# Kernel optimization log

Measured on AMD Instinct MI355X. Metric: run time of the kernel, lower is better.

## Reference

```python
import jax, jax.numpy as jnp
import numpy as np

SIGMA = 1.0
N_DOCS = 10_000_000
N_SAMPLED = 8192  # n = ceil(sqrt(random_pairs)), random_pairs = 67108864


def setup_inputs() -> dict:
    key = jax.random.key(0)
    k1, k2, k3 = jax.random.split(key, 3)
    scores = jax.random.normal(k1, (N_DOCS, 1), dtype=jnp.float32)
    target = jax.random.randint(k2, (N_DOCS,), 0, 5, dtype=jnp.int32)
    random_docs = jax.random.randint(k3, (N_SAMPLED,), 0, N_DOCS, dtype=jnp.int32)
    return {"scores": scores, "target": target, "random_docs": random_docs}


def reference(scores, target, random_docs):
    # Gather sampled docs' targets and scores.
    t = target[random_docs].astype(jnp.float32)   # [n]
    s = scores[random_docs, 0]                    # [n]
    # S_ij = sign(target_i - target_j)  (the if/elif/else ladder in the source)
    S = jnp.sign(t[:, None] - t[None, :])         # [n, n]
    # Source bug preserved: z_j = s_i.detach(), so calc_p(z_i, z_j) = sigmoid(0) = 0.5 exactly.
    # lambda_ij = sigma * (0.5 * (1 - S) - 0.5). (i == j pairs contribute 0 since S = 0.)
    lam = SIGMA * (0.5 * (1.0 - S) - 0.5)         # [n, n]
    row = jnp.sum(lam, axis=1)                    # sum_j lambda_ij for each sampled i
    # Source bug preserved: lambda_i is never reset across the outer loop -> cumulative sum.
    cum = jnp.cumsum(row)                         # [n]
    # loss = sum_k cum_lambda[k] * s_{i_k}; lambdas are detached (constants w.r.t. grad).
    loss = jnp.sum(jax.lax.stop_gradient(cum) * s)
    return loss.reshape(1)
```

## Files before the change

### kernel.cpp

```cpp
#include <hip/hip_runtime.h>

#define NS   8192
#define NB   64
#define T1   128
#define RECW 16

__device__ __forceinline__ unsigned fnv11(const unsigned* w, unsigned seed) {
    unsigned h = seed;
    #pragma unroll
    for (int i = 0; i < 11; ++i) h = (h ^ w[i]) * 16777619u;
    return h;
}

__global__ __launch_bounds__(T1) void k_fused(
    const float* __restrict__ scores,
    const int*   __restrict__ target,
    const int*   __restrict__ docs,
    unsigned*    __restrict__ ws,
    float*       __restrict__ out)
{
    const int tid  = threadIdx.x;
    const int b    = blockIdx.x;
    const int lane = tid & 63;
    const int wave = tid >> 6;

    if (b != 0) {
        const int   g = b - 1;
        const int   d = docs[g * T1 + tid];
        const int   t = target[d];
        const float s = scores[d];

        float incl = s;
        #pragma unroll
        for (int off = 1; off < 64; off <<= 1) {
            const float v = __shfl_up(incl, off, 64);
            if (lane >= off) incl += v;
        }
        const float wexcl = incl - s;
        const float wsum  = __shfl(incl, 63, 64);

        float cntw[5], pqw[5];
        #pragma unroll
        for (int v = 0; v < 5; ++v) {
            const unsigned long long m = __ballot(t == v);
            cntw[v] = (float)__popcll(m);
            float x = (t == v) ? wexcl : 0.0f;
            #pragma unroll
            for (int off = 32; off > 0; off >>= 1)
                x += __shfl_down(x, off, 64);
            pqw[v] = x;
        }

        __shared__ float l1[11];
        if (wave == 1 && lane == 0) {
            #pragma unroll
            for (int v = 0; v < 5; ++v) { l1[v] = cntw[v]; l1[5 + v] = pqw[v]; }
            l1[10] = wsum;
        }
        __syncthreads();

        if (wave == 0 && lane == 0) {
            unsigned w[11];
            #pragma unroll
            for (int v = 0; v < 5; ++v) {
                const float c = cntw[v] + l1[v];
                const float p = pqw[v] + l1[5 + v] + wsum * l1[v];
                w[v]     = __float_as_uint(c);
                w[5 + v] = __float_as_uint(p);
            }
            w[10] = __float_as_uint(wsum + l1[10]);
            const unsigned h1 = fnv11(w, 2166136261u);
            const unsigned h2 = fnv11(w, 0x9E3779B9u);
            unsigned* rec = ws + g * RECW;
            #pragma unroll
            for (int i = 0; i < 11; ++i)
                __hip_atomic_store(&rec[i], w[i], __ATOMIC_RELAXED,
                                   __HIP_MEMORY_SCOPE_AGENT);
            __hip_atomic_store(&rec[11], h1, __ATOMIC_RELAXED,
                               __HIP_MEMORY_SCOPE_AGENT);
            __hip_atomic_store(&rec[12], h2, __ATOMIC_RELAXED,
                               __HIP_MEMORY_SCOPE_AGENT);
        }
        return;
    }

    if (wave != 0) return;

    unsigned w[11];
    const unsigned* rec = ws + lane * RECW;
    bool ok = false;
    do {
        if (!ok) {
            #pragma unroll
            for (int i = 0; i < 11; ++i)
                w[i] = __hip_atomic_load(&rec[i], __ATOMIC_RELAXED,
                                         __HIP_MEMORY_SCOPE_AGENT);
            const unsigned c1 = __hip_atomic_load(&rec[11], __ATOMIC_ACQUIRE,
                                                  __HIP_MEMORY_SCOPE_AGENT);
            const unsigned c2 = __hip_atomic_load(&rec[12], __ATOMIC_ACQUIRE,
                                                  __HIP_MEMORY_SCOPE_AGENT);
            ok = (c1 == fnv11(w, 2166136261u)) &&
                 (c2 == fnv11(w, 0x9E3779B9u));
        }
        if (!__all(ok)) __builtin_amdgcn_s_sleep(1);
    } while (!__all(ok));

    float cnt[5], pq[5];
    #pragma unroll
    for (int v = 0; v < 5; ++v) {
        cnt[v] = __uint_as_float(w[v]);
        pq[v]  = __uint_as_float(w[5 + v]);
    }
    const float ssum = __uint_as_float(w[10]);

    float bincl = ssum;
    #pragma unroll
    for (int off = 1; off < 64; off <<= 1) {
        const float v = __shfl_up(bincl, off, 64);
        if (lane >= off) bincl += v;
    }
    const float S_total = __shfl(bincl, 63, 64);
    const float preoff  = bincl - ssum;

    double Q[5], C[5];
    #pragma unroll
    for (int v = 0; v < 5; ++v) {
        Q[v] = (double)cnt[v] * (double)(S_total - preoff) - (double)pq[v];
        C[v] = (double)cnt[v];
    }

    #pragma unroll
    for (int v = 0; v < 5; ++v) {
        #pragma unroll
        for (int off = 32; off > 0; off >>= 1) {
            Q[v] += __shfl_down(Q[v], off, 64);
            C[v] += __shfl_down(C[v], off, 64);
        }
    }

    if (lane == 0) {
        double loss = 0.0;
        #pragma unroll
        for (int ww = 0; ww < 5; ++ww) {
            double lo = 0.0, hi = 0.0;
            #pragma unroll
            for (int v = 0; v < 5; ++v) {
                if (v < ww) lo += Q[v];
                if (v > ww) hi += Q[v];
            }
            loss += C[ww] * (lo - hi);
        }
        out[0] = (float)(0.5 * loss);
    }
}

extern "C" void kernel_launch(void* const* d_in, const int* in_sizes, int n_in,
                              void* d_out, int out_size, void* d_ws, size_t ws_size,
                              hipStream_t stream) {
    const float* scores = (const float*)d_in[0];
    const int*   target = (const int*)d_in[1];
    const int*   docs   = (const int*)d_in[2];
    float*       out    = (float*)d_out;
    unsigned*    ws     = (unsigned*)d_ws;

    k_fused<<<NB + 1, T1, 0, stream>>>(scores, target, docs, ws, out);
}
```

Baseline: 9.699 us.

## Emit per-wave records to drop block barrier; reduce in float in the final wave

Producer blocks now have each wave write its own partial record (128 records), which removes the shared-memory exchange and __syncthreads between the two waves of each block. The consumer wave polls two records per lane and combines them, and the hash-check loads are relaxed instead of acquire. The final cross-lane reductions use float with xor shuffles instead of double, keeping double only for the last combine. This trims barrier and double-precision shuffle latency on a latency-bound path, at the cost of twice the polling loads and some loss of precision in the float reductions.

After: 9.808 us. About the same (+1.1%).

```diff
diff --git a/kernel.cpp b/kernel.cpp
--- a/kernel.cpp
+++ b/kernel.cpp
@@ -3,6 +3,7 @@
 #define NS   8192
 #define NB   64
 #define T1   128
+#define NREC 128
 #define RECW 16
 
 __device__ __forceinline__ unsigned fnv11(const unsigned* w, unsigned seed) {
@@ -25,8 +26,8 @@
     const int wave = tid >> 6;
 
     if (b != 0) {
-        const int   g = b - 1;
-        const int   d = docs[g * T1 + tid];
+        const int   r = (b - 1) * 2 + wave;
+        const int   d = docs[r * 64 + lane];
         const int   t = target[d];
         const float s = scores[d];
 
@@ -51,27 +52,17 @@
             pqw[v] = x;
         }
 
-        __shared__ float l1[11];
-        if (wave == 1 && lane == 0) {
-            #pragma unroll
-            for (int v = 0; v < 5; ++v) { l1[v] = cntw[v]; l1[5 + v] = pqw[v]; }
-            l1[10] = wsum;
-        }
-        __syncthreads();
-
-        if (wave == 0 && lane == 0) {
+        if (lane == 0) {
             unsigned w[11];
             #pragma unroll
             for (int v = 0; v < 5; ++v) {
-                const float c = cntw[v] + l1[v];
-                const float p = pqw[v] + l1[5 + v] + wsum * l1[v];
-                w[v]     = __float_as_uint(c);
-                w[5 + v] = __float_as_uint(p);
+                w[v]     = __float_as_uint(cntw[v]);
+                w[5 + v] = __float_as_uint(pqw[v]);
             }
-            w[10] = __float_as_uint(wsum + l1[10]);
+            w[10] = __float_as_uint(wsum);
             const unsigned h1 = fnv11(w, 2166136261u);
             const unsigned h2 = fnv11(w, 0x9E3779B9u);
-            unsigned* rec = ws + g * RECW;
+            unsigned* rec = ws + r * RECW;
             #pragma unroll
             for (int i = 0; i < 11; ++i)
                 __hip_atomic_store(&rec[i], w[i], __ATOMIC_RELAXED,
@@ -86,32 +77,50 @@
 
     if (wave != 0) return;
 
-    unsigned w[11];
-    const unsigned* rec = ws + lane * RECW;
-    bool ok = false;
+    unsigned w0[11], w1[11];
+    const unsigned* r0 = ws + (2 * lane)     * RECW;
+    const unsigned* r1 = ws + (2 * lane + 1) * RECW;
+    bool ok0 = false, ok1 = false;
     do {
-        if (!ok) {
+        if (!ok0) {
             #pragma unroll
             for (int i = 0; i < 11; ++i)
-                w[i] = __hip_atomic_load(&rec[i], __ATOMIC_RELAXED,
-                                         __HIP_MEMORY_SCOPE_AGENT);
-            const unsigned c1 = __hip_atomic_load(&rec[11], __ATOMIC_ACQUIRE,
+                w0[i] = __hip_atomic_load(&r0[i], __ATOMIC_RELAXED,
+                                          __HIP_MEMORY_SCOPE_AGENT);
+            const unsigned c1 = __hip_atomic_load(&r0[11], __ATOMIC_RELAXED,
                                                   __HIP_MEMORY_SCOPE_AGENT);
-            const unsigned c2 = __hip_atomic_load(&rec[12], __ATOMIC_ACQUIRE,
+            const unsigned c2 = __hip_atomic_load(&r0[12], __ATOMIC_RELAXED,
                                                   __HIP_MEMORY_SCOPE_AGENT);
-            ok = (c1 == fnv11(w, 2166136261u)) &&
-                 (c2 == fnv11(w, 0x9E3779B9u));
+            ok0 = (c1 == fnv11(w0, 2166136261u)) &&
+                  (c2 == fnv11(w0, 0x9E3779B9u));
         }
-        if (!__all(ok)) __builtin_amdgcn_s_sleep(1);
-    } while (!__all(ok));
+        if (!ok1) {
+            #pragma unroll
+            for (int i = 0; i < 11; ++i)
+                w1[i] = __hip_atomic_load(&r1[i], __ATOMIC_RELAXED,
+                                          __HIP_MEMORY_SCOPE_AGENT);
+            const unsigned c1 = __hip_atomic_load(&r1[11], __ATOMIC_RELAXED,
+                                                  __HIP_MEMORY_SCOPE_AGENT);
+            const unsigned c2 = __hip_atomic_load(&r1[12], __ATOMIC_RELAXED,
+                                                  __HIP_MEMORY_SCOPE_AGENT);
+            ok1 = (c1 == fnv11(w1, 2166136261u)) &&
+                  (c2 == fnv11(w1, 0x9E3779B9u));
+        }
+        if (!__all(ok0 && ok1)) __builtin_amdgcn_s_sleep(1);
+    } while (!__all(ok0 && ok1));
 
+    const float ws0 = __uint_as_float(w0[10]);
+    const float ws1 = __uint_as_float(w1[10]);
     float cnt[5], pq[5];
     #pragma unroll
     for (int v = 0; v < 5; ++v) {
-        cnt[v] = __uint_as_float(w[v]);
-        pq[v]  = __uint_as_float(w[5 + v]);
+        const float c0 = __uint_as_float(w0[v]);
+        const float c1v = __uint_as_float(w1[v]);
+        cnt[v] = c0 + c1v;
+        pq[v]  = __uint_as_float(w0[5 + v]) + __uint_as_float(w1[5 + v])
+               + ws0 * c1v;
     }
-    const float ssum = __uint_as_float(w[10]);
+    const float ssum = ws0 + ws1;
 
     float bincl = ssum;
     #pragma unroll
@@ -122,19 +131,18 @@
     const float S_total = __shfl(bincl, 63, 64);
     const float preoff  = bincl - ssum;
 
-    double Q[5], C[5];
+    float Q[5], C[5];
     #pragma unroll
     for (int v = 0; v < 5; ++v) {
-        Q[v] = (double)cnt[v] * (double)(S_total - preoff) - (double)pq[v];
-        C[v] = (double)cnt[v];
+        Q[v] = cnt[v] * (S_total - preoff) - pq[v];
+        C[v] = cnt[v];
     }
-
     #pragma unroll
     for (int v = 0; v < 5; ++v) {
         #pragma unroll
         for (int off = 32; off > 0; off >>= 1) {
-            Q[v] += __shfl_down(Q[v], off, 64);
-            C[v] += __shfl_down(C[v], off, 64);
+            Q[v] += __shfl_xor(Q[v], off, 64);
+            C[v] += __shfl_xor(C[v], off, 64);
         }
     }
 
@@ -145,10 +153,10 @@
             double lo = 0.0, hi = 0.0;
             #pragma unroll
             for (int v = 0; v < 5; ++v) {
-                if (v < ww) lo += Q[v];
-                if (v > ww) hi += Q[v];
+                if (v < ww) lo += (double)Q[v];
+                if (v > ww) hi += (double)Q[v];
             }
-            loss += C[ww] * (lo - hi);
+            loss += (double)C[ww] * (lo - hi);
         }
         out[0] = (float)(0.5 * loss);
     }
```
